# Performance work log

Measured on AMD Instinct MI355X. Metric: run time of the kernel, lower is better.

Reference implementation:

```python
import jax, jax.numpy as jnp
import numpy as np

B, NF, H = 1024, 64, 512


def setup_inputs() -> dict:
    key = jax.random.key(0)
    ks = jax.random.split(key, 12)
    sc_in2 = 1.0 / np.sqrt(2 * H)
    sc_in1 = 1.0 / np.sqrt(H)
    inp = {
        "field_vectors": jax.random.normal(ks[0], (B, NF, H), dtype=jnp.float32),
        # and_fusion: Linear(2H->H), ReLU, Linear(H->H)
        "and_W1": jax.random.uniform(ks[1], (2 * H, H), jnp.float32, -sc_in2, sc_in2),
        "and_b1": jax.random.uniform(ks[2], (H,), jnp.float32, -sc_in2, sc_in2),
        "and_W2": jax.random.uniform(ks[3], (H, H), jnp.float32, -sc_in1, sc_in1),
        "and_b2": jax.random.uniform(ks[4], (H,), jnp.float32, -sc_in1, sc_in1),
        # or_fusion: Linear(2H->H), ReLU, Linear(H->H)
        "or_W1": jax.random.uniform(ks[5], (2 * H, H), jnp.float32, -sc_in2, sc_in2),
        "or_b1": jax.random.uniform(ks[6], (H,), jnp.float32, -sc_in2, sc_in2),
        "or_W2": jax.random.uniform(ks[7], (H, H), jnp.float32, -sc_in1, sc_in1),
        "or_b2": jax.random.uniform(ks[8], (H,), jnp.float32, -sc_in1, sc_in1),
        # not_transform: Linear(H->H), Tanh
        "not_W": jax.random.uniform(ks[9], (H, H), jnp.float32, -sc_in1, sc_in1),
        "not_b": jax.random.uniform(ks[10], (H,), jnp.float32, -sc_in1, sc_in1),
        # Disjoint index structure so the torch skip-set logic is a no-op:
        # 'and' pairs use fields 0..31, 'or' pairs use 32..47, leftovers 48..63.
        "not_idx": 48 + jnp.arange(8, dtype=jnp.int32),
        "and_pairs": jnp.arange(32, dtype=jnp.int32).reshape(16, 2),
        "or_pairs": (32 + jnp.arange(16, dtype=jnp.int32)).reshape(8, 2),
        "leftover_idx": 48 + jnp.arange(16, dtype=jnp.int32),
    }
    return inp


def _mlp2(x, W1, b1, W2, b2):
    # Linear -> ReLU -> Linear
    return jax.nn.relu(x @ W1 + b1) @ W2 + b2


def reference(field_vectors, and_W1, and_b1, and_W2, and_b2,
              or_W1, or_b1, or_W2, or_b2, not_W, not_b,
              not_idx, and_pairs, or_pairs, leftover_idx):
    # In-place 'not' transform on selected fields (Tanh(Linear))
    fv = field_vectors.at[:, not_idx].set(
        jnp.tanh(field_vectors[:, not_idx] @ not_W + not_b))
    # Gather (i, j) pairs, concat along feature dim -> [B, P, 2H]
    cat_and = jnp.concatenate([fv[:, and_pairs[:, 0]], fv[:, and_pairs[:, 1]]], axis=-1)
    fused_and = _mlp2(cat_and, and_W1, and_b1, and_W2, and_b2)  # [B, 16, H]
    cat_or = jnp.concatenate([fv[:, or_pairs[:, 0]], fv[:, or_pairs[:, 1]]], axis=-1)
    fused_or = _mlp2(cat_or, or_W1, or_b1, or_W2, or_b2)  # [B, 8, H]
    # Stack order matches torch loop: and results, or results, untouched fields
    return jnp.concatenate([fused_and, fused_or, fv[:, leftover_idx]], axis=1)
```

## Files before the change

kernel.cpp:

```cpp
#include <hip/hip_runtime.h>
#include <hip/hip_bf16.h>
#include <math.h>

typedef __attribute__((ext_vector_type(8))) __bf16 bf16x8;
typedef __attribute__((ext_vector_type(4))) float f32x4;

__device__ __forceinline__ unsigned short f2bf(float f) {
    union { float f; unsigned u; } v; v.f = f;
    unsigned r = v.u + 0x7fffu + ((v.u >> 16) & 1u);
    return (unsigned short)(r >> 16);
}
__device__ __forceinline__ unsigned int pk(float a, float b) {
    union { float f; unsigned u; } x, y; x.f = a; y.f = b;
    unsigned ra = (x.u + 0x7fffu + ((x.u >> 16) & 1u)) >> 16;
    unsigned rb = (y.u + 0x7fffu + ((y.u >> 16) & 1u)) & 0xffff0000u;
    return ra | rb;
}

__device__ __forceinline__ void gl2lds16(const unsigned short* g, unsigned short* l) {
    __builtin_amdgcn_global_load_lds(
        (const __attribute__((address_space(1))) unsigned int*)(g),
        (__attribute__((address_space(3))) unsigned int*)(l), 16, 0, 0);
}

struct PrepArgs {
    const float* fv;
    unsigned short *and_At, *or_At, *not_At;
    const int *and_pairs, *or_pairs, *not_idx, *lidx;
    float* out;
    const float* W[5];
    unsigned short* WT[5];
    int N[5];
    int tstart[6];
};

__global__ __launch_bounds__(256) void prep_kernel(PrepArgs a) {
    __shared__ float tile[64][65];
    const int blk = blockIdx.x;
    const int tid = threadIdx.x;

    if (blk < 448) {
        int m = 0;
        while (blk >= a.tstart[m + 1]) m++;
        const float* src = a.W[m];
        unsigned short* dst = a.WT[m];
        const int N = a.N[m];
        const int t = blk - a.tstart[m];
        const int ntn = N >> 6;
        const int tk = t / ntn, tn = t % ntn;
        const int c = tid & 63, r0 = tid >> 6;
        #pragma unroll
        for (int r = r0; r < 64; r += 4)
            tile[r][c] = src[(size_t)(tk * 64 + r) * N + tn * 64 + c];
        __syncthreads();
        const int l = tid & 63;
        #pragma unroll
        for (int fi = tid >> 6; fi < 8; fi += 4) {
            const int ktl = fi & 1, cgl = fi >> 1;
            const int kt = tk * 2 + ktl, cg = tn * 4 + cgl;
            const int kb = ktl * 32 + (l >> 4) * 8;
            const int nb = cgl * 16 + (l & 15);
            uint4 o;
            o.x = pk(tile[kb + 0][nb], tile[kb + 1][nb]);
            o.y = pk(tile[kb + 2][nb], tile[kb + 3][nb]);
            o.z = pk(tile[kb + 4][nb], tile[kb + 5][nb]);
            o.w = pk(tile[kb + 6][nb], tile[kb + 7][nb]);
            ((uint4*)dst)[((size_t)kt * 32 + cg) * 64 + l] = o;
        }
        return;
    }

    const int t = (blk - 448) * 256 + tid;
    const int lane = tid & 63;
    const size_t e = (size_t)t * 8;
    const int c = (int)(e & 511);
    const int f = (int)((e >> 9) & 63);
    const int b = (int)(e >> 15);
    const float4 v0 = *(const float4*)(a.fv + e);
    const float4 v1 = *(const float4*)(a.fv + e + 4);
    const int am = (lane < 32) ? a.and_pairs[lane] : -1;
    const int om = (lane < 16) ? a.or_pairs[lane]  : -1;
    const int nm = (lane <  8) ? a.not_idx[lane]   : -1;
    const int lm = (lane < 16) ? a.lidx[lane]      : -1;
    const unsigned long long ba = __ballot(am == f);
    const unsigned long long bo = __ballot(om == f);
    const unsigned long long bn = __ballot(nm == f);
    const unsigned long long bl = __ballot(lm == f);

    uint4 o;
    o.x = pk(v0.x, v0.y); o.y = pk(v0.z, v0.w);
    o.z = pk(v1.x, v1.y); o.w = pk(v1.z, v1.w);
    const int c8 = lane;
    const int kc = c8 & 3;

    if (ba) {
        const int j = (int)__builtin_ctzll(ba);
        const int m = b * 16 + (j >> 1);
        const int kt = (j & 1) * 16 + (c8 >> 2);
        const int r = m & 63;
        const int l = ((r & 15) << 2) | (kc ^ (r & 3));
        *(uint4*)(a.and_At +
            (((((size_t)(m >> 6) * 32 + kt) << 2) | (unsigned)(r >> 4)) << 9) +
            (l << 3)) = o;
    }
    if (bo) {
        const int j = (int)__builtin_ctzll(bo);
        const int m = b * 8 + (j >> 1);
        const int kt = (j & 1) * 16 + (c8 >> 2);
        const int r = m & 63;
        const int l = ((r & 15) << 2) | (kc ^ (r & 3));
        *(uint4*)(a.or_At +
            (((((size_t)(m >> 6) * 32 + kt) << 2) | (unsigned)(r >> 4)) << 9) +
            (l << 3)) = o;
    }
    if (bn) {
        const int i = (int)__builtin_ctzll(bn);
        const int m = b * 8 + i;
        const int kt = c8 >> 2;
        const int r = m & 63;
        const int l = ((r & 15) << 2) | (kc ^ (r & 3));
        *(uint4*)(a.not_At +
            (((((size_t)(m >> 6) * 16 + kt) << 2) | (unsigned)(r >> 4)) << 9) +
            (l << 3)) = o;
    }
    if (bl && !bn) {
        const int ls = (int)__builtin_ctzll(bl);
        float* d = a.out + ((size_t)b * 40 + 24 + ls) * 512 + c;
        *(float4*)(d)     = v0;
        *(float4*)(d + 4) = v1;
    }
}

#define LOADB(DST, WTP, K0)                                                  \
    _Pragma("unroll") for (int ni = 0; ni < 4; ni++)                         \
        DST[ni] = *(const bf16x8*)((WTP) +                                   \
            ((((size_t)(K0) >> 5) * 32 + cg0 + ni) << 9) + (lane << 3));

#define MMAC(BF, AF)                                                         \
    _Pragma("unroll") for (int mi = 0; mi < 4; mi++)                         \
    _Pragma("unroll") for (int ni = 0; ni < 4; ni++)                         \
        acc[mi][ni] = __builtin_amdgcn_mfma_f32_16x16x32_bf16(               \
            AF[mi], BF[ni], acc[mi][ni], 0, 0, 0);

#define AFRD(AF, BUF)                                                        \
    _Pragma("unroll") for (int mi = 0; mi < 4; mi++)                         \
        AF[mi] = *(const bf16x8*)&As[(BUF) * 2048 +                          \
                                     (mi * 16 + ln15) * 32 + xsel];

#define FBAR()                                                               \
    asm volatile("s_waitcnt vmcnt(4) lgkmcnt(0)" ::: "memory");              \
    asm volatile("s_barrier" ::: "memory");

template <int P, int K1, int PATH, int QBASE>
__device__ __forceinline__ void fused_seg(
    const unsigned short* __restrict__ At,
    const unsigned short* __restrict__ W1T,
    const float* __restrict__ b1,
    const unsigned short* __restrict__ W2T,
    const float* __restrict__ b2,
    float* __restrict__ out,
    const int* __restrict__ nidx,
    const int* __restrict__ leftover,
    int local,
    unsigned short* As, unsigned short* hid) {

    const int tid  = threadIdx.x;
    const int lane = tid & 63, w = tid >> 6;
    const int ln15 = lane & 15;
    const int kq   = lane >> 4;
    const int wn   = w * 64;
    const int cg0  = w * 4;
    const int m0   = local * 64;
    constexpr int NTK = K1 / 32;

    const unsigned short* abase =
        At + (size_t)local * NTK * 2048 + ((w & 3) << 9) + (lane << 3);
    auto stageA = [&](int buf, int t) {
        gl2lds16(abase + (size_t)t * 2048, &As[buf * 2048 + (w & 3) * 512]);
    };
    const int xsel = (kq ^ (lane & 3)) * 8;

    f32x4 acc[4][4];
    #pragma unroll
    for (int mi = 0; mi < 4; mi++)
        #pragma unroll
        for (int ni = 0; ni < 4; ni++)
            acc[mi][ni] = f32x4{0.f, 0.f, 0.f, 0.f};

    bf16x8 bA[4], bB[4];

    if (w < 4) { stageA(0, 0); stageA(1, 1); }
    __builtin_amdgcn_sched_barrier(0);
    LOADB(bA, W1T, 0);

    for (int h = 0; h < NTK; h += 2) {
        bf16x8 af[4];
        FBAR();
        if (h + 1 < NTK) { LOADB(bB, W1T, (h + 1) * 32); }
        __builtin_amdgcn_sched_barrier(0);
        if (w < 4 && h + 2 < NTK) stageA((h + 2) & 3, h + 2);
        __builtin_amdgcn_sched_barrier(0);
        AFRD(af, h & 3);
        MMAC(bA, af);
        __builtin_amdgcn_sched_barrier(0);
        FBAR();
        if (h + 2 < NTK) { LOADB(bA, W1T, (h + 2) * 32); }
        __builtin_amdgcn_sched_barrier(0);
        if (w < 4 && h + 3 < NTK) stageA((h + 3) & 3, h + 3);
        __builtin_amdgcn_sched_barrier(0);
        AFRD(af, (h + 1) & 3);
        MMAC(bB, af);
        __builtin_amdgcn_sched_barrier(0);
    }

    if constexpr (PATH == 2) {
        int qmap[8];
        #pragma unroll
        for (int i = 0; i < 8; i++) {
            const int f = nidx[i];
            int q = 24;
            for (int l = 0; l < 16; l++)
                if (leftover[l] == f) q = 24 + l;
            qmap[i] = q;
        }
        #pragma unroll
        for (int ni = 0; ni < 4; ni++) {
            const int n = wn + ni * 16 + ln15;
            const float bv = b1[n];
            #pragma unroll
            for (int mi = 0; mi < 4; mi++)
                #pragma unroll
                for (int j = 0; j < 4; j++) {
                    const int r = mi * 16 + kq * 4 + j;
                    const int m = m0 + r;
                    const int b = m >> 3, i = m & 7;
                    out[((size_t)b * 40 + qmap[i]) * 512 + n] =
                        tanhf(acc[mi][ni][j] + bv);
                }
        }
        return;
    }

    #pragma unroll
    for (int ni = 0; ni < 4; ni++) {
        const int n  = wn + ni * 16 + ln15;
        const float bv = b1[n];
        const int c8 = n >> 3;
        const int cl = (n & 7) * 2;
        #pragma unroll
        for (int mi = 0; mi < 4; mi++)
            #pragma unroll
            for (int j = 0; j < 4; j++) {
                const int r = mi * 16 + kq * 4 + j;
                float v = acc[mi][ni][j] + bv;
                v = v > 0.f ? v : 0.f;
                *(unsigned short*)((char*)hid + r * 1024 +
                                   ((c8 ^ (r & 7)) * 16) + cl) = f2bf(v);
            }
    }
    #pragma unroll
    for (int mi = 0; mi < 4; mi++)
        #pragma unroll
        for (int ni = 0; ni < 4; ni++)
            acc[mi][ni] = f32x4{0.f, 0.f, 0.f, 0.f};
    __syncthreads();

    LOADB(bA, W2T, 0);
    for (int t2 = 0; t2 < 16; t2 += 2) {
        bf16x8 af[4];
        LOADB(bB, W2T, (t2 + 1) * 32);
        #pragma unroll
        for (int mi = 0; mi < 4; mi++) {
            const int r = mi * 16 + ln15;
            const int c8 = t2 * 4 + kq;
            af[mi] = *(const bf16x8*)((char*)hid + r * 1024 +
                                      ((c8 ^ (r & 7)) * 16));
        }
        MMAC(bA, af);
        if (t2 + 2 < 16) { LOADB(bA, W2T, (t2 + 2) * 32); }
        #pragma unroll
        for (int mi = 0; mi < 4; mi++) {
            const int r = mi * 16 + ln15;
            const int c8 = (t2 + 1) * 4 + kq;
            af[mi] = *(const bf16x8*)((char*)hid + r * 1024 +
                                      ((c8 ^ (r & 7)) * 16));
        }
        MMAC(bB, af);
    }

    #pragma unroll
    for (int ni = 0; ni < 4; ni++) {
        const int n  = wn + ni * 16 + ln15;
        const float bv = b2[n];
        #pragma unroll
        for (int mi = 0; mi < 4; mi++)
            #pragma unroll
            for (int j = 0; j < 4; j++) {
                const int r = mi * 16 + kq * 4 + j;
                const int m = m0 + r;
                const int b = m / P, p = m % P;
                out[((size_t)b * 40 + QBASE + p) * 512 + n] =
                    acc[mi][ni][j] + bv;
            }
    }
}

struct FArgs {
    const unsigned short *and_At, *or_At, *not_At;
    const unsigned short *and_W1T, *and_W2T, *or_W1T, *or_W2T, *not_WT;
    const int *not_idx, *leftover;
    const float *and_b1, *and_b2, *or_b1, *or_b2, *not_b;
    float* out;
};

__global__ __launch_bounds__(512, 4) void fused_phase(FArgs a) {
    __shared__ __align__(16) unsigned short As[4 * 64 * 32];
    __shared__ __align__(16) unsigned short hid[64 * 512];
    const int blk = blockIdx.x;
    if (blk < 256)
        fused_seg<16, 1024, 0, 0>(a.and_At, a.and_W1T, a.and_b1,
                                  a.and_W2T, a.and_b2, a.out,
                                  nullptr, nullptr, blk, As, hid);
    else if (blk < 384)
        fused_seg<8, 1024, 0, 16>(a.or_At, a.or_W1T, a.or_b1,
                                  a.or_W2T, a.or_b2, a.out,
                                  nullptr, nullptr, blk - 256, As, hid);
    else
        fused_seg<8, 512, 2, 24>(a.not_At, a.not_WT, a.not_b,
                                 nullptr, nullptr, a.out,
                                 a.not_idx, a.leftover, blk - 384, As, hid);
}

extern "C" void kernel_launch(void* const* d_in, const int* in_sizes, int n_in,
                              void* d_out, int out_size, void* d_ws, size_t ws_size,
                              hipStream_t stream) {
    const float* fv       = (const float*)d_in[0];
    const float* and_W1   = (const float*)d_in[1];
    const float* and_b1   = (const float*)d_in[2];
    const float* and_W2   = (const float*)d_in[3];
    const float* and_b2   = (const float*)d_in[4];
    const float* or_W1    = (const float*)d_in[5];
    const float* or_b1    = (const float*)d_in[6];
    const float* or_W2    = (const float*)d_in[7];
    const float* or_b2    = (const float*)d_in[8];
    const float* not_W    = (const float*)d_in[9];
    const float* not_b    = (const float*)d_in[10];
    const int* not_idx    = (const int*)d_in[11];
    const int* and_pairs  = (const int*)d_in[12];
    const int* or_pairs   = (const int*)d_in[13];
    const int* leftover   = (const int*)d_in[14];
    float* out = (float*)d_out;
    char* ws = (char*)d_ws;

    unsigned short* and_At  = (unsigned short*)(ws);
    unsigned short* or_At   = (unsigned short*)(ws + 33554432);
    unsigned short* not_At  = (unsigned short*)(ws + 50331648);
    unsigned short* and_W1T = (unsigned short*)(ws + 58720256);
    unsigned short* or_W1T  = (unsigned short*)(ws + 59768832);
    unsigned short* and_W2T = (unsigned short*)(ws + 60817408);
    unsigned short* or_W2T  = (unsigned short*)(ws + 61341696);
    unsigned short* not_WT  = (unsigned short*)(ws + 61865984);

    PrepArgs pa;
    pa.fv = fv; pa.out = out;
    pa.and_At = and_At; pa.or_At = or_At; pa.not_At = not_At;
    pa.and_pairs = and_pairs; pa.or_pairs = or_pairs;
    pa.not_idx = not_idx; pa.lidx = leftover;
    pa.W[0] = and_W1; pa.WT[0] = and_W1T; pa.N[0] = 512;
    pa.W[1] = or_W1;  pa.WT[1] = or_W1T;  pa.N[1] = 512;
    pa.W[2] = and_W2; pa.WT[2] = and_W2T; pa.N[2] = 512;
    pa.W[3] = or_W2;  pa.WT[3] = or_W2T;  pa.N[3] = 512;
    pa.W[4] = not_W;  pa.WT[4] = not_WT;  pa.N[4] = 512;
    pa.tstart[0] = 0;   pa.tstart[1] = 128; pa.tstart[2] = 256;
    pa.tstart[3] = 320; pa.tstart[4] = 384; pa.tstart[5] = 448;
    prep_kernel<<<dim3(448 + 16384), dim3(256), 0, stream>>>(pa);

    FArgs fa;
    fa.and_At = and_At; fa.or_At = or_At; fa.not_At = not_At;
    fa.and_W1T = and_W1T; fa.and_W2T = and_W2T;
    fa.or_W1T = or_W1T;   fa.or_W2T = or_W2T;   fa.not_WT = not_WT;
    fa.not_idx = not_idx; fa.leftover = leftover;
    fa.and_b1 = and_b1; fa.and_b2 = and_b2;
    fa.or_b1 = or_b1;   fa.or_b2 = or_b2;   fa.not_b = not_b;
    fa.out = out;
    fused_phase<<<dim3(512), dim3(512), 0, stream>>>(fa);
}
```

Before: 299.6 us.

## Load A fragments directly from global into registers, dropping LDS staging

```diff
diff --git a/kernel.cpp b/kernel.cpp
--- a/kernel.cpp
+++ b/kernel.cpp
@@ -15,12 +15,6 @@
     unsigned ra = (x.u + 0x7fffu + ((x.u >> 16) & 1u)) >> 16;
     unsigned rb = (y.u + 0x7fffu + ((y.u >> 16) & 1u)) & 0xffff0000u;
     return ra | rb;
-}
-
-__device__ __forceinline__ void gl2lds16(const unsigned short* g, unsigned short* l) {
-    __builtin_amdgcn_global_load_lds(
-        (const __attribute__((address_space(1))) unsigned int*)(g),
-        (__attribute__((address_space(3))) unsigned int*)(l), 16, 0, 0);
 }
 
 struct PrepArgs {
@@ -98,7 +92,7 @@
         const int m = b * 16 + (j >> 1);
         const int kt = (j & 1) * 16 + (c8 >> 2);
         const int r = m & 63;
-        const int l = ((r & 15) << 2) | (kc ^ (r & 3));
+        const int l = (kc << 4) | (r & 15);
         *(uint4*)(a.and_At +
             (((((size_t)(m >> 6) * 32 + kt) << 2) | (unsigned)(r >> 4)) << 9) +
             (l << 3)) = o;
@@ -108,7 +102,7 @@
         const int m = b * 8 + (j >> 1);
         const int kt = (j & 1) * 16 + (c8 >> 2);
         const int r = m & 63;
-        const int l = ((r & 15) << 2) | (kc ^ (r & 3));
+        const int l = (kc << 4) | (r & 15);
         *(uint4*)(a.or_At +
             (((((size_t)(m >> 6) * 32 + kt) << 2) | (unsigned)(r >> 4)) << 9) +
             (l << 3)) = o;
@@ -118,7 +112,7 @@
         const int m = b * 8 + i;
         const int kt = c8 >> 2;
         const int r = m & 63;
-        const int l = ((r & 15) << 2) | (kc ^ (r & 3));
+        const int l = (kc << 4) | (r & 15);
         *(uint4*)(a.not_At +
             (((((size_t)(m >> 6) * 16 + kt) << 2) | (unsigned)(r >> 4)) << 9) +
             (l << 3)) = o;
@@ -136,20 +130,16 @@
         DST[ni] = *(const bf16x8*)((WTP) +                                   \
             ((((size_t)(K0) >> 5) * 32 + cg0 + ni) << 9) + (lane << 3));
 
+#define LOADA(DST, ATP, K0)                                                  \
+    _Pragma("unroll") for (int mi = 0; mi < 4; mi++)                         \
+        DST[mi] = *(const bf16x8*)((ATP) +                                   \
+            ((((size_t)(K0) >> 5) * 4 + mi) << 9) + (lane << 3));
+
 #define MMAC(BF, AF)                                                         \
     _Pragma("unroll") for (int mi = 0; mi < 4; mi++)                         \
     _Pragma("unroll") for (int ni = 0; ni < 4; ni++)                         \
         acc[mi][ni] = __builtin_amdgcn_mfma_f32_16x16x32_bf16(               \
             AF[mi], BF[ni], acc[mi][ni], 0, 0, 0);
-
-#define AFRD(AF, BUF)                                                        \
-    _Pragma("unroll") for (int mi = 0; mi < 4; mi++)                         \
-        AF[mi] = *(const bf16x8*)&As[(BUF) * 2048 +                          \
-                                     (mi * 16 + ln15) * 32 + xsel];
-
-#define FBAR()                                                               \
-    asm volatile("s_waitcnt vmcnt(4) lgkmcnt(0)" ::: "memory");              \
-    asm volatile("s_barrier" ::: "memory");
 
 template <int P, int K1, int PATH, int QBASE>
 __device__ __forceinline__ void fused_seg(
@@ -162,7 +152,7 @@
     const int* __restrict__ nidx,
     const int* __restrict__ leftover,
     int local,
-    unsigned short* As, unsigned short* hid) {
+    unsigned short* hid) {
 
     const int tid  = threadIdx.x;
     const int lane = tid & 63, w = tid >> 6;
@@ -173,12 +163,7 @@
     const int m0   = local * 64;
     constexpr int NTK = K1 / 32;
 
-    const unsigned short* abase =
-        At + (size_t)local * NTK * 2048 + ((w & 3) << 9) + (lane << 3);
-    auto stageA = [&](int buf, int t) {
-        gl2lds16(abase + (size_t)t * 2048, &As[buf * 2048 + (w & 3) * 512]);
-    };
-    const int xsel = (kq ^ (lane & 3)) * 8;
+    const unsigned short* At0 = At + (size_t)local * NTK * 2048;
 
     f32x4 acc[4][4];
     #pragma unroll
@@ -187,30 +172,16 @@
         for (int ni = 0; ni < 4; ni++)
             acc[mi][ni] = f32x4{0.f, 0.f, 0.f, 0.f};
 
-    bf16x8 bA[4], bB[4];
-
-    if (w < 4) { stageA(0, 0); stageA(1, 1); }
-    __builtin_amdgcn_sched_barrier(0);
-    LOADB(bA, W1T, 0);
-
+    bf16x8 aA[4], aB[4], bA[4];
+
+    LOADA(aA, At0, 0);
     for (int h = 0; h < NTK; h += 2) {
-        bf16x8 af[4];
-        FBAR();
-        if (h + 1 < NTK) { LOADB(bB, W1T, (h + 1) * 32); }
-        __builtin_amdgcn_sched_barrier(0);
-        if (w < 4 && h + 2 < NTK) stageA((h + 2) & 3, h + 2);
-        __builtin_amdgcn_sched_barrier(0);
-        AFRD(af, h & 3);
-        MMAC(bA, af);
-        __builtin_amdgcn_sched_barrier(0);
-        FBAR();
-        if (h + 2 < NTK) { LOADB(bA, W1T, (h + 2) * 32); }
-        __builtin_amdgcn_sched_barrier(0);
-        if (w < 4 && h + 3 < NTK) stageA((h + 3) & 3, h + 3);
-        __builtin_amdgcn_sched_barrier(0);
-        AFRD(af, (h + 1) & 3);
-        MMAC(bB, af);
-        __builtin_amdgcn_sched_barrier(0);
+        LOADA(aB, At0, (h + 1) * 32);
+        LOADB(bA, W1T, h * 32);
+        MMAC(bA, aA);
+        if (h + 2 < NTK) { LOADA(aA, At0, (h + 2) * 32); }
+        LOADB(bA, W1T, (h + 1) * 32);
+        MMAC(bA, aB);
     }
 
     if constexpr (PATH == 2) {
@@ -265,6 +236,7 @@
             acc[mi][ni] = f32x4{0.f, 0.f, 0.f, 0.f};
     __syncthreads();
 
+    bf16x8 bB[4];
     LOADB(bA, W2T, 0);
     for (int t2 = 0; t2 < 16; t2 += 2) {
         bf16x8 af[4];
@@ -314,21 +286,20 @@
 };
 
 __global__ __launch_bounds__(512, 4) void fused_phase(FArgs a) {
-    __shared__ __align__(16) unsigned short As[4 * 64 * 32];
     __shared__ __align__(16) unsigned short hid[64 * 512];
     const int blk = blockIdx.x;
     if (blk < 256)
         fused_seg<16, 1024, 0, 0>(a.and_At, a.and_W1T, a.and_b1,
                                   a.and_W2T, a.and_b2, a.out,
-                                  nullptr, nullptr, blk, As, hid);
+                                  nullptr, nullptr, blk, hid);
     else if (blk < 384)
         fused_seg<8, 1024, 0, 16>(a.or_At, a.or_W1T, a.or_b1,
                                   a.or_W2T, a.or_b2, a.out,
-                                  nullptr, nullptr, blk - 256, As, hid);
+                                  nullptr, nullptr, blk - 256, hid);
     else
         fused_seg<8, 512, 2, 24>(a.not_At, a.not_WT, a.not_b,
                                  nullptr, nullptr, a.out,
-                                 a.not_idx, a.leftover, blk - 384, As, hid);
+                                 a.not_idx, a.leftover, blk - 384, hid);
 }
 
 extern "C" void kernel_launch(void* const* d_in, const int* in_sizes, int n_in,
```

After: 322.4 us. 7.6% more time.

## Restructure activation prep to gather only needed fields per batch via LDS

Applied to the files above, without the earlier changes.

```diff
diff --git a/kernel.cpp b/kernel.cpp
--- a/kernel.cpp
+++ b/kernel.cpp
@@ -22,6 +22,8 @@
         (const __attribute__((address_space(1))) unsigned int*)(g),
         (__attribute__((address_space(3))) unsigned int*)(l), 16, 0, 0);
 }
+
+#define LROW 520
 
 struct PrepArgs {
     const float* fv;
@@ -35,11 +37,12 @@
 };
 
 __global__ __launch_bounds__(256) void prep_kernel(PrepArgs a) {
-    __shared__ float tile[64][65];
+    __shared__ __align__(16) unsigned short smem[56 * LROW];
     const int blk = blockIdx.x;
     const int tid = threadIdx.x;
 
     if (blk < 448) {
+        float (*tile)[65] = (float(*)[65])smem;
         int m = 0;
         while (blk >= a.tstart[m + 1]) m++;
         const float* src = a.W[m];
@@ -70,64 +73,70 @@
         return;
     }
 
-    const int t = (blk - 448) * 256 + tid;
-    const int lane = tid & 63;
-    const size_t e = (size_t)t * 8;
-    const int c = (int)(e & 511);
-    const int f = (int)((e >> 9) & 63);
-    const int b = (int)(e >> 15);
-    const float4 v0 = *(const float4*)(a.fv + e);
-    const float4 v1 = *(const float4*)(a.fv + e + 4);
-    const int am = (lane < 32) ? a.and_pairs[lane] : -1;
-    const int om = (lane < 16) ? a.or_pairs[lane]  : -1;
-    const int nm = (lane <  8) ? a.not_idx[lane]   : -1;
-    const int lm = (lane < 16) ? a.lidx[lane]      : -1;
-    const unsigned long long ba = __ballot(am == f);
-    const unsigned long long bo = __ballot(om == f);
-    const unsigned long long bn = __ballot(nm == f);
-    const unsigned long long bl = __ballot(lm == f);
-
-    uint4 o;
-    o.x = pk(v0.x, v0.y); o.y = pk(v0.z, v0.w);
-    o.z = pk(v1.x, v1.y); o.w = pk(v1.z, v1.w);
-    const int c8 = lane;
-    const int kc = c8 & 3;
-
-    if (ba) {
-        const int j = (int)__builtin_ctzll(ba);
-        const int m = b * 16 + (j >> 1);
-        const int kt = (j & 1) * 16 + (c8 >> 2);
-        const int r = m & 63;
-        const int l = ((r & 15) << 2) | (kc ^ (r & 3));
-        *(uint4*)(a.and_At +
-            (((((size_t)(m >> 6) * 32 + kt) << 2) | (unsigned)(r >> 4)) << 9) +
-            (l << 3)) = o;
-    }
-    if (bo) {
-        const int j = (int)__builtin_ctzll(bo);
-        const int m = b * 8 + (j >> 1);
-        const int kt = (j & 1) * 16 + (c8 >> 2);
-        const int r = m & 63;
-        const int l = ((r & 15) << 2) | (kc ^ (r & 3));
-        *(uint4*)(a.or_At +
-            (((((size_t)(m >> 6) * 32 + kt) << 2) | (unsigned)(r >> 4)) << 9) +
-            (l << 3)) = o;
-    }
-    if (bn) {
-        const int i = (int)__builtin_ctzll(bn);
-        const int m = b * 8 + i;
-        const int kt = c8 >> 2;
-        const int r = m & 63;
-        const int l = ((r & 15) << 2) | (kc ^ (r & 3));
-        *(uint4*)(a.not_At +
-            (((((size_t)(m >> 6) * 16 + kt) << 2) | (unsigned)(r >> 4)) << 9) +
-            (l << 3)) = o;
-    }
-    if (bl && !bn) {
-        const int ls = (int)__builtin_ctzll(bl);
-        float* d = a.out + ((size_t)b * 40 + 24 + ls) * 512 + c;
-        *(float4*)(d)     = v0;
-        *(float4*)(d + 4) = v1;
+    const int b    = blk - 448;
+    const int lane = tid & 63, w = tid >> 6;
+
+    for (int s = w; s < 56; s += 4) {
+        int f;
+        if (s < 32)      f = a.and_pairs[2 * (s & 15) + (s >> 4)];
+        else if (s < 48) f = a.or_pairs[2 * ((s - 32) & 7) + ((s - 32) >> 3)];
+        else             f = a.not_idx[s - 48];
+        const float* src = a.fv + ((size_t)b * 64 + f) * 512 + lane * 8;
+        const float4 v0 = *(const float4*)(src);
+        const float4 v1 = *(const float4*)(src + 4);
+        uint4 o;
+        o.x = pk(v0.x, v0.y); o.y = pk(v0.z, v0.w);
+        o.z = pk(v1.x, v1.y); o.w = pk(v1.z, v1.w);
+        *(uint4*)(smem + s * LROW + lane * 8) = o;
+    }
+    for (int ls = w; ls < 16; ls += 4) {
+        const int f = a.lidx[ls];
+        int isnot = 0;
+        #pragma unroll
+        for (int i = 0; i < 8; i++) isnot |= (a.not_idx[i] == f);
+        if (isnot) continue;
+        const float* s = a.fv + ((size_t)b * 64 + f) * 512 + lane * 8;
+        float* d = a.out + ((size_t)b * 40 + 24 + ls) * 512 + lane * 8;
+        *(float4*)(d)     = *(const float4*)(s);
+        *(float4*)(d + 4) = *(const float4*)(s + 4);
+    }
+    __syncthreads();
+
+    {
+        const int p  = lane >> 2;
+        const int kc = (lane & 3) ^ (p & 3);
+        for (int kt = w; kt < 32; kt += 4) {
+            const int h = kt >> 4, kslot = kt & 15;
+            const uint4 v = *(const uint4*)(smem + (p + 16 * h) * LROW +
+                                            kslot * 32 + kc * 8);
+            ((uint4*)a.and_At)[((((size_t)(b >> 2) * 32 + kt) << 2) |
+                               (unsigned)(b & 3)) * 64 + lane] = v;
+        }
+    }
+    {
+        const int p = (lane >> 2) - ((b & 1) * 8);
+        if (p >= 0 && p < 8) {
+            const int kc = (lane & 3) ^ (p & 3);
+            for (int kt = w; kt < 32; kt += 4) {
+                const int h = kt >> 4, kslot = kt & 15;
+                const uint4 v = *(const uint4*)(smem + (32 + p + 8 * h) * LROW +
+                                                kslot * 32 + kc * 8);
+                ((uint4*)a.or_At)[((((size_t)(b >> 3) * 32 + kt) << 2) |
+                                  (unsigned)((b & 7) >> 1)) * 64 + lane] = v;
+            }
+        }
+    }
+    {
+        const int i = (lane >> 2) - ((b & 1) * 8);
+        if (i >= 0 && i < 8) {
+            const int kc = (lane & 3) ^ (i & 3);
+            for (int kt = w; kt < 16; kt += 4) {
+                const uint4 v = *(const uint4*)(smem + (48 + i) * LROW +
+                                                kt * 32 + kc * 8);
+                ((uint4*)a.not_At)[((((size_t)(b >> 3) * 16 + kt) << 2) |
+                                   (unsigned)((b & 7) >> 1)) * 64 + lane] = v;
+            }
+        }
     }
 }
 
@@ -373,7 +382,7 @@
     pa.W[4] = not_W;  pa.WT[4] = not_WT;  pa.N[4] = 512;
     pa.tstart[0] = 0;   pa.tstart[1] = 128; pa.tstart[2] = 256;
     pa.tstart[3] = 320; pa.tstart[4] = 384; pa.tstart[5] = 448;
-    prep_kernel<<<dim3(448 + 16384), dim3(256), 0, stream>>>(pa);
+    prep_kernel<<<dim3(448 + 1024), dim3(256), 0, stream>>>(pa);
 
     FArgs fa;
     fa.and_At = and_At; fa.or_At = or_At; fa.not_At = not_At;
```

New measurement: 321.5 us. 1.07x slower.

## Fuse activation gather and bf16 packing into the fused GEMM kernel

Applied to the files above, without the earlier changes.

```diff
diff --git a/kernel.cpp b/kernel.cpp
--- a/kernel.cpp
+++ b/kernel.cpp
@@ -23,10 +23,9 @@
         (__attribute__((address_space(3))) unsigned int*)(l), 16, 0, 0);
 }
 
-struct PrepArgs {
+struct WArgs {
     const float* fv;
-    unsigned short *and_At, *or_At, *not_At;
-    const int *and_pairs, *or_pairs, *not_idx, *lidx;
+    const int *not_idx, *leftover;
     float* out;
     const float* W[5];
     unsigned short* WT[5];
@@ -34,100 +33,55 @@
     int tstart[6];
 };
 
-__global__ __launch_bounds__(256) void prep_kernel(PrepArgs a) {
+__global__ __launch_bounds__(256) void wprep_kernel(WArgs a) {
     __shared__ float tile[64][65];
     const int blk = blockIdx.x;
     const int tid = threadIdx.x;
 
-    if (blk < 448) {
-        int m = 0;
-        while (blk >= a.tstart[m + 1]) m++;
-        const float* src = a.W[m];
-        unsigned short* dst = a.WT[m];
-        const int N = a.N[m];
-        const int t = blk - a.tstart[m];
-        const int ntn = N >> 6;
-        const int tk = t / ntn, tn = t % ntn;
-        const int c = tid & 63, r0 = tid >> 6;
-        #pragma unroll
-        for (int r = r0; r < 64; r += 4)
-            tile[r][c] = src[(size_t)(tk * 64 + r) * N + tn * 64 + c];
-        __syncthreads();
-        const int l = tid & 63;
-        #pragma unroll
-        for (int fi = tid >> 6; fi < 8; fi += 4) {
-            const int ktl = fi & 1, cgl = fi >> 1;
-            const int kt = tk * 2 + ktl, cg = tn * 4 + cgl;
-            const int kb = ktl * 32 + (l >> 4) * 8;
-            const int nb = cgl * 16 + (l & 15);
-            uint4 o;
-            o.x = pk(tile[kb + 0][nb], tile[kb + 1][nb]);
-            o.y = pk(tile[kb + 2][nb], tile[kb + 3][nb]);
-            o.z = pk(tile[kb + 4][nb], tile[kb + 5][nb]);
-            o.w = pk(tile[kb + 6][nb], tile[kb + 7][nb]);
-            ((uint4*)dst)[((size_t)kt * 32 + cg) * 64 + l] = o;
-        }
+    if (blk >= 448) {
+        const int t = (blk - 448) * 256 + tid;
+        const size_t e = (size_t)t * 8;
+        const int c  = (int)(e & 511);
+        const int ls = (int)((e >> 9) & 15);
+        const int b  = (int)(e >> 13);
+        const int f  = a.leftover[ls];
+        int isnot = 0;
+        #pragma unroll
+        for (int i = 0; i < 8; i++) isnot |= (a.not_idx[i] == f);
+        if (isnot) return;
+        const float* s = a.fv + ((size_t)b * 64 + f) * 512 + c;
+        float* d = a.out + ((size_t)b * 40 + 24 + ls) * 512 + c;
+        *(float4*)(d)     = *(const float4*)(s);
+        *(float4*)(d + 4) = *(const float4*)(s + 4);
         return;
     }
 
-    const int t = (blk - 448) * 256 + tid;
-    const int lane = tid & 63;
-    const size_t e = (size_t)t * 8;
-    const int c = (int)(e & 511);
-    const int f = (int)((e >> 9) & 63);
-    const int b = (int)(e >> 15);
-    const float4 v0 = *(const float4*)(a.fv + e);
-    const float4 v1 = *(const float4*)(a.fv + e + 4);
-    const int am = (lane < 32) ? a.and_pairs[lane] : -1;
-    const int om = (lane < 16) ? a.or_pairs[lane]  : -1;
-    const int nm = (lane <  8) ? a.not_idx[lane]   : -1;
-    const int lm = (lane < 16) ? a.lidx[lane]      : -1;
-    const unsigned long long ba = __ballot(am == f);
-    const unsigned long long bo = __ballot(om == f);
-    const unsigned long long bn = __ballot(nm == f);
-    const unsigned long long bl = __ballot(lm == f);
-
-    uint4 o;
-    o.x = pk(v0.x, v0.y); o.y = pk(v0.z, v0.w);
-    o.z = pk(v1.x, v1.y); o.w = pk(v1.z, v1.w);
-    const int c8 = lane;
-    const int kc = c8 & 3;
-
-    if (ba) {
-        const int j = (int)__builtin_ctzll(ba);
-        const int m = b * 16 + (j >> 1);
-        const int kt = (j & 1) * 16 + (c8 >> 2);
-        const int r = m & 63;
-        const int l = ((r & 15) << 2) | (kc ^ (r & 3));
-        *(uint4*)(a.and_At +
-            (((((size_t)(m >> 6) * 32 + kt) << 2) | (unsigned)(r >> 4)) << 9) +
-            (l << 3)) = o;
-    }
-    if (bo) {
-        const int j = (int)__builtin_ctzll(bo);
-        const int m = b * 8 + (j >> 1);
-        const int kt = (j & 1) * 16 + (c8 >> 2);
-        const int r = m & 63;
-        const int l = ((r & 15) << 2) | (kc ^ (r & 3));
-        *(uint4*)(a.or_At +
-            (((((size_t)(m >> 6) * 32 + kt) << 2) | (unsigned)(r >> 4)) << 9) +
-            (l << 3)) = o;
-    }
-    if (bn) {
-        const int i = (int)__builtin_ctzll(bn);
-        const int m = b * 8 + i;
-        const int kt = c8 >> 2;
-        const int r = m & 63;
-        const int l = ((r & 15) << 2) | (kc ^ (r & 3));
-        *(uint4*)(a.not_At +
-            (((((size_t)(m >> 6) * 16 + kt) << 2) | (unsigned)(r >> 4)) << 9) +
-            (l << 3)) = o;
-    }
-    if (bl && !bn) {
-        const int ls = (int)__builtin_ctzll(bl);
-        float* d = a.out + ((size_t)b * 40 + 24 + ls) * 512 + c;
-        *(float4*)(d)     = v0;
-        *(float4*)(d + 4) = v1;
+    int m = 0;
+    while (blk >= a.tstart[m + 1]) m++;
+    const float* src = a.W[m];
+    unsigned short* dst = a.WT[m];
+    const int N = a.N[m];
+    const int t = blk - a.tstart[m];
+    const int ntn = N >> 6;
+    const int tk = t / ntn, tn = t % ntn;
+    const int c = tid & 63, r0 = tid >> 6;
+    #pragma unroll
+    for (int r = r0; r < 64; r += 4)
+        tile[r][c] = src[(size_t)(tk * 64 + r) * N + tn * 64 + c];
+    __syncthreads();
+    const int l = tid & 63;
+    #pragma unroll
+    for (int fi = tid >> 6; fi < 8; fi += 4) {
+        const int ktl = fi & 1, cgl = fi >> 1;
+        const int kt = tk * 2 + ktl, cg = tn * 4 + cgl;
+        const int kb = ktl * 32 + (l >> 4) * 8;
+        const int nb = cgl * 16 + (l & 15);
+        uint4 o;
+        o.x = pk(tile[kb + 0][nb], tile[kb + 1][nb]);
+        o.y = pk(tile[kb + 2][nb], tile[kb + 3][nb]);
+        o.z = pk(tile[kb + 4][nb], tile[kb + 5][nb]);
+        o.w = pk(tile[kb + 6][nb], tile[kb + 7][nb]);
+        ((uint4*)dst)[((size_t)kt * 32 + cg) * 64 + l] = o;
     }
 }
 
@@ -153,13 +107,14 @@
 
 template <int P, int K1, int PATH, int QBASE>
 __device__ __forceinline__ void fused_seg(
-    const unsigned short* __restrict__ At,
+    const float* __restrict__ fv,
+    const int* __restrict__ idx,
+    unsigned short* __restrict__ At,
     const unsigned short* __restrict__ W1T,
     const float* __restrict__ b1,
     const unsigned short* __restrict__ W2T,
     const float* __restrict__ b2,
     float* __restrict__ out,
-    const int* __restrict__ nidx,
     const int* __restrict__ leftover,
     int local,
     unsigned short* As, unsigned short* hid) {
@@ -173,8 +128,43 @@
     const int m0   = local * 64;
     constexpr int NTK = K1 / 32;
 
-    const unsigned short* abase =
-        At + (size_t)local * NTK * 2048 + ((w & 3) << 9) + (lane << 3);
+    unsigned short* const slice = At + (size_t)local * NTK * 2048;
+
+    {
+        const int r = tid >> 3;
+        const int j = tid & 7;
+        const int m = m0 + r;
+        const float *f0p, *f1p;
+        if constexpr (PATH == 0) {
+            const int b = m / P, p = m % P;
+            f0p = fv + ((size_t)b * 64 + idx[2 * p]) * 512;
+            f1p = fv + ((size_t)b * 64 + idx[2 * p + 1]) * 512;
+        } else {
+            const int b = m >> 3, i = m & 7;
+            f0p = fv + ((size_t)b * 64 + idx[i]) * 512;
+            f1p = f0p;
+        }
+        const int lbase = (r & 15) << 2;
+        constexpr int NIT = NTK / 2;
+        #pragma unroll
+        for (int it = 0; it < NIT; it++) {
+            const int c8 = it * 8 + j;
+            const int kt = c8 >> 2;
+            const int kc = c8 & 3;
+            const float* src = (c8 >= 64 ? f1p + (c8 - 64) * 8 : f0p + c8 * 8);
+            const float4 v0 = *(const float4*)(src);
+            const float4 v1 = *(const float4*)(src + 4);
+            uint4 o;
+            o.x = pk(v0.x, v0.y); o.y = pk(v0.z, v0.w);
+            o.z = pk(v1.x, v1.y); o.w = pk(v1.z, v1.w);
+            *(uint4*)(slice + (((size_t)kt * 4 + (r >> 4)) << 9) +
+                      ((lbase | (kc ^ (r & 3))) << 3)) = o;
+        }
+        asm volatile("s_waitcnt vmcnt(0)" ::: "memory");
+        __syncthreads();
+    }
+
+    const unsigned short* abase = slice + ((w & 3) << 9) + (lane << 3);
     auto stageA = [&](int buf, int t) {
         gl2lds16(abase + (size_t)t * 2048, &As[buf * 2048 + (w & 3) * 512]);
     };
@@ -217,7 +207,7 @@
         int qmap[8];
         #pragma unroll
         for (int i = 0; i < 8; i++) {
-            const int f = nidx[i];
+            const int f = idx[i];
             int q = 24;
             for (int l = 0; l < 16; l++)
                 if (leftover[l] == f) q = 24 + l;
@@ -306,9 +296,10 @@
 }
 
 struct FArgs {
-    const unsigned short *and_At, *or_At, *not_At;
+    const float* fv;
+    unsigned short *and_At, *or_At, *not_At;
     const unsigned short *and_W1T, *and_W2T, *or_W1T, *or_W2T, *not_WT;
-    const int *not_idx, *leftover;
+    const int *and_pairs, *or_pairs, *not_idx, *leftover;
     const float *and_b1, *and_b2, *or_b1, *or_b2, *not_b;
     float* out;
 };
@@ -318,17 +309,17 @@
     __shared__ __align__(16) unsigned short hid[64 * 512];
     const int blk = blockIdx.x;
     if (blk < 256)
-        fused_seg<16, 1024, 0, 0>(a.and_At, a.and_W1T, a.and_b1,
-                                  a.and_W2T, a.and_b2, a.out,
-                                  nullptr, nullptr, blk, As, hid);
+        fused_seg<16, 1024, 0, 0>(a.fv, a.and_pairs, a.and_At,
+                                  a.and_W1T, a.and_b1, a.and_W2T, a.and_b2,
+                                  a.out, nullptr, blk, As, hid);
     else if (blk < 384)
-        fused_seg<8, 1024, 0, 16>(a.or_At, a.or_W1T, a.or_b1,
-                                  a.or_W2T, a.or_b2, a.out,
-                                  nullptr, nullptr, blk - 256, As, hid);
+        fused_seg<8, 1024, 0, 16>(a.fv, a.or_pairs, a.or_At,
+                                  a.or_W1T, a.or_b1, a.or_W2T, a.or_b2,
+                                  a.out, nullptr, blk - 256, As, hid);
     else
-        fused_seg<8, 512, 2, 24>(a.not_At, a.not_WT, a.not_b,
-                                 nullptr, nullptr, a.out,
-                                 a.not_idx, a.leftover, blk - 384, As, hid);
+        fused_seg<8, 512, 2, 24>(a.fv, a.not_idx, a.not_At,
+                                 a.not_WT, a.not_b, nullptr, nullptr,
+                                 a.out, a.leftover, blk - 384, As, hid);
 }
 
 extern "C" void kernel_launch(void* const* d_in, const int* in_sizes, int n_in,
@@ -361,25 +352,25 @@
     unsigned short* or_W2T  = (unsigned short*)(ws + 61341696);
     unsigned short* not_WT  = (unsigned short*)(ws + 61865984);
 
-    PrepArgs pa;
-    pa.fv = fv; pa.out = out;
-    pa.and_At = and_At; pa.or_At = or_At; pa.not_At = not_At;
-    pa.and_pairs = and_pairs; pa.or_pairs = or_pairs;
-    pa.not_idx = not_idx; pa.lidx = leftover;
-    pa.W[0] = and_W1; pa.WT[0] = and_W1T; pa.N[0] = 512;
-    pa.W[1] = or_W1;  pa.WT[1] = or_W1T;  pa.N[1] = 512;
-    pa.W[2] = and_W2; pa.WT[2] = and_W2T; pa.N[2] = 512;
-    pa.W[3] = or_W2;  pa.WT[3] = or_W2T;  pa.N[3] = 512;
-    pa.W[4] = not_W;  pa.WT[4] = not_WT;  pa.N[4] = 512;
-    pa.tstart[0] = 0;   pa.tstart[1] = 128; pa.tstart[2] = 256;
-    pa.tstart[3] = 320; pa.tstart[4] = 384; pa.tstart[5] = 448;
-    prep_kernel<<<dim3(448 + 16384), dim3(256), 0, stream>>>(pa);
+    WArgs wa;
+    wa.fv = fv; wa.out = out;
+    wa.not_idx = not_idx; wa.leftover = leftover;
+    wa.W[0] = and_W1; wa.WT[0] = and_W1T; wa.N[0] = 512;
+    wa.W[1] = or_W1;  wa.WT[1] = or_W1T;  wa.N[1] = 512;
+    wa.W[2] = and_W2; wa.WT[2] = and_W2T; wa.N[2] = 512;
+    wa.W[3] = or_W2;  wa.WT[3] = or_W2T;  wa.N[3] = 512;
+    wa.W[4] = not_W;  wa.WT[4] = not_WT;  wa.N[4] = 512;
+    wa.tstart[0] = 0;   wa.tstart[1] = 128; wa.tstart[2] = 256;
+    wa.tstart[3] = 320; wa.tstart[4] = 384; wa.tstart[5] = 448;
+    wprep_kernel<<<dim3(448 + 4096), dim3(256), 0, stream>>>(wa);
 
     FArgs fa;
+    fa.fv = fv;
     fa.and_At = and_At; fa.or_At = or_At; fa.not_At = not_At;
     fa.and_W1T = and_W1T; fa.and_W2T = and_W2T;
     fa.or_W1T = or_W1T;   fa.or_W2T = or_W2T;   fa.not_WT = not_WT;
-    fa.not_idx = not_idx; fa.leftover = leftover;
+    fa.and_pairs = and_pairs; fa.or_pairs = or_pairs; fa.not_idx = not_idx;
+    fa.leftover = leftover;
     fa.and_b1 = and_b1; fa.and_b2 = and_b2;
     fa.or_b1 = or_b1;   fa.or_b2 = or_b2;   fa.not_b = not_b;
     fa.out = out;
```

After: 316.9 us. +5.8%, slower.
